# Performance work log

Measured on AMD Instinct MI355X. Metric: run time of the kernel, lower is better.

## Reference

```python
import jax, jax.numpy as jnp
import numpy as np

B, T, I, H, C, L = 64, 256, 256, 1024, 1000, 2


def setup_inputs() -> dict:
    key = jax.random.key(0)
    ks = jax.random.split(key, 10)
    stdv = 1.0 / np.sqrt(H)
    u = lambda k, shape: jax.random.uniform(k, shape, jnp.float32, -stdv, stdv)
    return {
        "x": jax.random.normal(ks[0], (B, T, I), jnp.float32),
        # gate order: g (tanh), i, f, o — stacked on leading axis
        "W0x": u(ks[1], (4, I, H)),
        "W0h": u(ks[2], (4, H, H)),
        "b0": u(ks[3], (4, H)),
        "W1x": u(ks[4], (4, H, H)),
        "W1h": u(ks[5], (4, H, H)),
        "b1": u(ks[6], (4, H)),
        "Wo": u(ks[7], (H, C)),
        "bo": u(ks[8], (C,)),
    }


def _cell(x, h, c, Wx, Wh, b):
    # z: [4, B, H] — one fused contraction for the 4 gates
    z = jnp.einsum('bi,gih->gbh', x, Wx) + jnp.einsum('bh,ghk->gbk', h, Wh) + b[:, None, :]
    g = jnp.tanh(z[0])
    i = jax.nn.sigmoid(z[1])
    f = jax.nn.sigmoid(z[2])
    o = jax.nn.sigmoid(z[3])
    c_new = g * i + c * f
    h_new = jnp.tanh(c_new) * o
    return h_new, c_new


def reference(x, W0x, W0h, b0, W1x, W1h, b1, Wo, bo):
    xt = jnp.transpose(x, (1, 0, 2))  # [T, B, I] like x.permute(1,0,2)
    zeros = jnp.zeros((B, H), x.dtype)
    init = (zeros, zeros, zeros, zeros)  # h0, c0, h1, c1

    def step(carry, x_t):
        h0, c0, h1, c1 = carry
        h0, c0 = _cell(x_t, h0, c0, W0x, W0h, b0)
        h1, c1 = _cell(h0, h1, c1, W1x, W1h, b1)
        return (h0, c0, h1, c1), None

    (h0, c0, h1, c1), _ = jax.lax.scan(step, init, xt)
    return jnp.matmul(h1, Wo) + bo
```

## Files before the change

kernel.cpp:

```cpp
#include <hip/hip_runtime.h>
#include <cstddef>

#define B_  64
#define T_  256
#define I_  256
#define H_  1024
#define C_  1000
#define BH_ (B_ * H_)
#define SLOTS_B_ 24

typedef _Float16 f16;
typedef __attribute__((ext_vector_type(8))) _Float16 f16x8;
typedef __attribute__((ext_vector_type(4))) float f32x4;

__device__ __forceinline__ float sigmoid_(float v) { return 1.0f / (1.0f + __expf(-v)); }
__device__ __forceinline__ float tanh_(float v) {
  float e = __expf(-2.0f * fabsf(v));
  float t = (1.0f - e) / (1.0f + e);
  return copysignf(t, v);
}

__device__ __forceinline__ void storeH2(f16* p, float a, float b) {
  union { f16 h[2]; unsigned u; } pk;
  pk.h[0] = (f16)a; pk.h[1] = (f16)b;
  __hip_atomic_store((unsigned*)p, pk.u, __ATOMIC_RELAXED, __HIP_MEMORY_SCOPE_AGENT);
}


__device__ __forceinline__ unsigned ldS(unsigned* p) {
  return __hip_atomic_load(p, __ATOMIC_RELAXED, __HIP_MEMORY_SCOPE_AGENT);
}

__device__ __forceinline__ void waitCtr8(unsigned* base, unsigned tgt) {
  int g = 0;
  for (;;) {
    unsigned mn = 0xffffffffu;
#pragma unroll
    for (int j = 0; j < 8; ++j) {
      unsigned v = ldS(base + j * 32);
      mn = (v < mn) ? v : mn;
    }
    if (mn >= tgt) break;
    __builtin_amdgcn_s_sleep(1);
    if (++g > (1 << 17)) break;
  }
}

template<bool IS_L1>
__device__ __forceinline__ void role_main(
    const f16* __restrict__ x16,
    const float* __restrict__ Wx, const float* __restrict__ Wh,
    const float* __restrict__ bias,
    f16* __restrict__ h0hist, f16* __restrict__ h1hist,
    unsigned* sync, int bid, int nslots, int fmask, int lagD,
    float* zbAll, float* cLDS, float* biasLDS)
{
  constexpr int NKT = IS_L1 ? 16 : 10;
  constexpr int KX  = IS_L1 ? 1024 : 256;

  const int tid  = threadIdx.x;
  const int wv   = tid >> 6;
  const int nh   = wv >> 2;
  const int kq   = wv & 3;
  const int lane = tid & 63;
  const int c16  = lane & 15;
  const int quad = lane >> 4;
  const int rr7  = bid & 127;
  const int mgroup  = rr7 & 1;
  const int ubase   = (rr7 >> 1) * 16;
  const int rowbase = mgroup * 32;

  const int sub = (rr7 >> 1) & 7;
  unsigned* ctrC0 = sync + ((0 * 2 + mgroup) * 8) * 32;
  unsigned* ctrC1 = sync + ((1 * 2 + mgroup) * 8) * 32;
  unsigned* ctrOwn = IS_L1 ? ctrC1 : ctrC0;
  unsigned* arrLine = ctrOwn + sub * 32;

  auto kmap = [&](int ii) -> int {
    if (!IS_L1) return (ii < 2) ? (kq * 2 + ii) * 32 : 256 + (kq * 8 + (ii - 2)) * 32;
    else        return (ii < 8) ? (kq * 8 + ii) * 32 : 1024 + (kq * 8 + (ii - 8)) * 32;
  };

  if (tid < 64) biasLDS[tid] = bias[(size_t)(tid >> 4) * H_ + ubase + (tid & 15)];
  cLDS[tid] = 0.0f;

  f16x8 Wreg[2][NKT];
  {
    f16* zpan = (f16*)zbAll + wv * 1024;
#pragma unroll
    for (int ii = 0; ii < NKT; ++ii) {
      const int kbase = kmap(ii);
#pragma unroll
      for (int rw = 0; rw < 16; ++rw) {
        const int krow  = rw * 2 + (lane >> 5);
        const int col32 = lane & 31;
        const int g = nh * 2 + (col32 >> 4);
        const int u = col32 & 15;
        const int k = kbase + krow;
        float wval = (k < KX) ? Wx[((size_t)g * KX + k) * H_ + ubase + u]
                              : Wh[((size_t)g * H_ + (k - KX)) * H_ + ubase + u];
        zpan[krow * 32 + col32] = (f16)wval;
      }
#pragma unroll
      for (int nt = 0; nt < 2; ++nt) {
        f16x8 f;
#pragma unroll
        for (int j = 0; j < 8; ++j)
          f[j] = zpan[(quad * 8 + j) * 32 + nt * 16 + c16];
        Wreg[nt][ii] = f;
      }
    }
  }
  __syncthreads();

  const int row0 = rowbase + c16;

#pragma unroll 1
  for (int p = 0; p <= T_; ++p) {
    const bool active = IS_L1 ? (p >= 1) : (p < T_);
    const int do_fence = (nslots == 2) ? 1
                        : ((fmask < 0) ? 0 : (((p & fmask) == fmask) ? 1 : 0));

    if (active) {
      const int sp  = p % nslots;
      const int spm = (p - 1 + nslots) % nslots;
      const int spp = (p + 1) % nslots;
      const f16* __restrict__ hA = h0hist + (size_t)sp * BH_;
      const f16* __restrict__ hB = h1hist + (size_t)spm * BH_;
      f16* __restrict__ hdst = IS_L1 ? (h1hist + (size_t)sp  * BH_)
                                     : (h0hist + (size_t)spp * BH_);

      f16x8 Abuf[8][2];
      auto loadTile = [&](int ii, int slot) {
        const int kb = kmap(ii) + quad * 8;
#pragma unroll
        for (int mt2 = 0; mt2 < 2; ++mt2) {
          const int row = row0 + mt2 * 16;
          const f16* src;
          if (!IS_L1) {
            src = (ii < 2) ? (x16 + ((size_t)row * T_ + p) * I_ + kb)
                           : (hA + (size_t)row * H_ + (kb - 256));
          } else {
            src = (ii < 8) ? (hA + (size_t)row * H_ + kb)
                           : (hB + (size_t)row * H_ + (kb - 1024));
          }
          Abuf[slot][mt2] = *(const f16x8*)src;
        }
      };

      f32x4 acc[2][2];
#pragma unroll
      for (int mt2 = 0; mt2 < 2; ++mt2)
#pragma unroll
        for (int nt = 0; nt < 2; ++nt)
          acc[mt2][nt] = (f32x4)0.0f;

      auto mfma4 = [&](int slot, int ii) {
        const f16x8 a0 = Abuf[slot][0];
        const f16x8 a1 = Abuf[slot][1];
        acc[0][0] = __builtin_amdgcn_mfma_f32_16x16x32_f16(a0, Wreg[0][ii], acc[0][0], 0, 0, 0);
        acc[0][1] = __builtin_amdgcn_mfma_f32_16x16x32_f16(a0, Wreg[1][ii], acc[0][1], 0, 0, 0);
        acc[1][0] = __builtin_amdgcn_mfma_f32_16x16x32_f16(a1, Wreg[0][ii], acc[1][0], 0, 0, 0);
        acc[1][1] = __builtin_amdgcn_mfma_f32_16x16x32_f16(a1, Wreg[1][ii], acc[1][1], 0, 0, 0);
      };

      if (!IS_L1) {
        loadTile(0, 0); loadTile(1, 1);
        mfma4(0, 0); mfma4(1, 1);
        if (tid == 0) {
          waitCtr8(ctrC0, 8u * (unsigned)p);
          if (lagD >= 0 && p > lagD) waitCtr8(ctrC1, 8u * (unsigned)(p - lagD));
          if (do_fence) __builtin_amdgcn_fence(__ATOMIC_ACQUIRE, "agent");
        }
        __syncthreads();
#pragma unroll
        for (int ii = 2; ii < 10; ++ii) loadTile(ii, ii - 2);
#pragma unroll
        for (int ii = 2; ii < 10; ++ii) mfma4(ii - 2, ii);
      } else {
        if (tid == 0) {
          waitCtr8(ctrC0, 8u * (unsigned)p);
          if (do_fence) __builtin_amdgcn_fence(__ATOMIC_ACQUIRE, "agent");
        }
        __syncthreads();
#pragma unroll
        for (int ii = 0; ii < 8; ++ii) loadTile(ii, ii);
#pragma unroll
        for (int ii = 0; ii < 8; ++ii) mfma4(ii, ii);
        if (tid == 0) {
          waitCtr8(ctrC1, 8u * (unsigned)p);
          if (do_fence) __builtin_amdgcn_fence(__ATOMIC_ACQUIRE, "agent");
        }
        __syncthreads();
#pragma unroll
        for (int ii = 8; ii < 16; ++ii) loadTile(ii, ii - 8);
#pragma unroll
        for (int ii = 8; ii < 16; ++ii) mfma4(ii - 8, ii);
      }

      float* zw = zbAll + (nh * 4 + kq) * 1024;
#pragma unroll
      for (int mt2 = 0; mt2 < 2; ++mt2)
#pragma unroll
        for (int nt = 0; nt < 2; ++nt)
#pragma unroll
          for (int e = 0; e < 4; ++e)
            zw[(mt2 * 2 + nt) * 256 + (quad * 4 + e) * 16 + c16] = acc[mt2][nt][e];

      __syncthreads();

      {
        const int base = tid * 4;
        const int nh1  = base >> 10;
        const int off  = base & 1023;
        f32x4 s = (f32x4)0.0f;
#pragma unroll
        for (int q = 0; q < 4; ++q)
          s += *(const f32x4*)(zbAll + nh1 * 4096 + q * 1024 + off);
        const int nt1 = (off >> 8) & 1;
        const int c0  = off & 15;
        s += *(const f32x4*)(biasLDS + (nh1 * 2 + nt1) * 16 + c0);
        *(f32x4*)(zbAll + nh1 * 4096 + off) = s;
      }
      __syncthreads();

      {
        const int row = tid >> 4, u = tid & 15;
        const int mt2 = row >> 4, r16 = row & 15;
        const float z0 = zbAll[0 * 4096 + (mt2 * 2 + 0) * 256 + r16 * 16 + u];
        const float z1 = zbAll[0 * 4096 + (mt2 * 2 + 1) * 256 + r16 * 16 + u];
        const float z2 = zbAll[1 * 4096 + (mt2 * 2 + 0) * 256 + r16 * 16 + u];
        const float z3 = zbAll[1 * 4096 + (mt2 * 2 + 1) * 256 + r16 * 16 + u];
        const float cv = cLDS[tid];
        const float gt = tanh_(z0);
        const float iv = sigmoid_(z1);
        const float fv = sigmoid_(z2);
        const float ov = sigmoid_(z3);
        const float cn = gt * iv + cv * fv;
        cLDS[tid] = cn;
        const float hn = tanh_(cn) * ov;
        const float hn_hi = __shfl_down(hn, 1);
        if ((tid & 1) == 0)
          storeH2(hdst + (size_t)(rowbase + row) * H_ + ubase + u, hn, hn_hi);
      }
    }

    __syncthreads();
    if (tid == 0)
      __hip_atomic_fetch_add(arrLine, 1u, __ATOMIC_RELAXED, __HIP_MEMORY_SCOPE_AGENT);
  }
}

__global__ __launch_bounds__(512, 2)
void lstm_persistent(const f16* __restrict__ x16,
                     const float* __restrict__ W0x, const float* __restrict__ W0h, const float* __restrict__ b0,
                     const float* __restrict__ W1x, const float* __restrict__ W1h, const float* __restrict__ b1,
                     f16* h0hist, f16* h1hist, unsigned* sync,
                     int nslots, int fmask, int lagD)
{
  __shared__ float zbAll[8192];
  __shared__ float cLDS[512];
  __shared__ float biasLDS[64];
  const int bid = blockIdx.x;
  if (bid >= 128)
    role_main<true >(x16, W1x, W1h, b1, h0hist, h1hist, sync, bid, nslots, fmask, lagD, zbAll, cLDS, biasLDS);
  else
    role_main<false>(x16, W0x, W0h, b0, h0hist, h1hist, sync, bid, nslots, fmask, lagD, zbAll, cLDS, biasLDS);
}

__global__ void cvt_x(const float* __restrict__ xin, f16* __restrict__ xo)
{
  const int i = (blockIdx.x * 256 + threadIdx.x) * 8;
  const float4 a = *(const float4*)(xin + i);
  const float4 b = *(const float4*)(xin + i + 4);
  f16x8 v;
  v[0] = (f16)a.x; v[1] = (f16)a.y; v[2] = (f16)a.z; v[3] = (f16)a.w;
  v[4] = (f16)b.x; v[5] = (f16)b.y; v[6] = (f16)b.z; v[7] = (f16)b.w;
  *(f16x8*)(xo + i) = v;
}

__global__ void out_gemm(const f16* __restrict__ h1,
                         const float* __restrict__ Wo, const float* __restrict__ bo,
                         float* __restrict__ out)
{
  __shared__ float ht[1024][8];
  const int tid = threadIdx.x;
  const int b0r = blockIdx.y * 4;
  for (int i = tid; i < 4096; i += 128) {
    const int rr = i >> 10, k = i & 1023;
    ht[k][rr] = (float)h1[(size_t)(b0r + rr) * H_ + k];
  }
  __syncthreads();
  const int c = blockIdx.x * 125 + tid;
  if (tid < 125) {
    float a0 = 0.f, a1 = 0.f, a2 = 0.f, a3 = 0.f;
#pragma unroll 4
    for (int k = 0; k < 1024; ++k) {
      const float w = Wo[(size_t)k * C_ + c];
      a0 += ht[k][0] * w;
      a1 += ht[k][1] * w;
      a2 += ht[k][2] * w;
      a3 += ht[k][3] * w;
    }
    const float bb = bo[c];
    out[(size_t)(b0r + 0) * C_ + c] = a0 + bb;
    out[(size_t)(b0r + 1) * C_ + c] = a1 + bb;
    out[(size_t)(b0r + 2) * C_ + c] = a2 + bb;
    out[(size_t)(b0r + 3) * C_ + c] = a3 + bb;
  }
}

extern "C" void kernel_launch(void* const* d_in, const int* in_sizes, int n_in,
                              void* d_out, int out_size, void* d_ws, size_t ws_size,
                              hipStream_t stream)
{
  const float* x   = (const float*)d_in[0];
  const float* W0x = (const float*)d_in[1];
  const float* W0h = (const float*)d_in[2];
  const float* b0  = (const float*)d_in[3];
  const float* W1x = (const float*)d_in[4];
  const float* W1h = (const float*)d_in[5];
  const float* b1  = (const float*)d_in[6];
  const float* Wo  = (const float*)d_in[7];
  const float* bo  = (const float*)d_in[8];

  const size_t slotB = (size_t)BH_ * sizeof(f16);
  const size_t xB    = (size_t)B_ * T_ * I_ * sizeof(f16);
  const size_t needA = 4096 + (size_t)2 * (T_ + 1) * slotB + xB;
  const size_t needB = 4096 + (size_t)2 * SLOTS_B_ * slotB + xB;
  int nslots, fmask, lagD;
  if (ws_size >= needA)      { nslots = T_ + 1;   fmask = -1; lagD = -1; }
  else if (ws_size >= needB) { nslots = SLOTS_B_; fmask = 15; lagD = 7;  }
  else                       { nslots = 2;        fmask = 0;  lagD = 0;  }
  const size_t histB = (size_t)nslots * slotB;

  unsigned* sync  = (unsigned*)d_ws;
  f16* h0hist = (f16*)((char*)d_ws + 4096);
  f16* h1hist = (f16*)((char*)h0hist + histB);
  f16* x16    = (f16*)((char*)h1hist + histB);

  hipMemsetAsync(d_ws, 0, 4096 + slotB, stream);
  hipMemsetAsync(h1hist, 0, slotB, stream);

  hipLaunchKernelGGL(cvt_x, dim3((B_ * T_ * I_) / (256 * 8)), dim3(256), 0, stream, x, x16);

  hipLaunchKernelGGL(lstm_persistent, dim3(256), dim3(512), 0, stream,
                     x16, W0x, W0h, b0, W1x, W1h, b1, h0hist, h1hist, sync,
                     nslots, fmask, lagD);

  f16* h1fin = h1hist + (size_t)(T_ % nslots) * BH_;
  hipLaunchKernelGGL(out_gemm, dim3(8, 16), dim3(128), 0, stream,
                     h1fin, Wo, bo, (float*)d_out);
}
```

Before: 2.542 ms.

## Merge layer-1 dual waits into one combined poll and deepen load buffering

Layer-1 blocks now wait on both the layer-0 and layer-1 counters in a single polling loop before any loads. They then issue all 16 tiles of loads using 10 register slots, instead of two wait/sync phases of 8. This removes one barrier and one wait per step and raises memory-level parallelism. The cost is that overlap of the first-half MFMAs with the second wait is lost. Polling now checks once before sleeping and uses exponential backoff, which adds wake-up latency when the wait runs long.

Result: slower. 2.718 ms (+6.9%).

```diff
diff --git a/kernel.cpp b/kernel.cpp
--- a/kernel.cpp
+++ b/kernel.cpp
@@ -31,18 +31,54 @@
   return __hip_atomic_load(p, __ATOMIC_RELAXED, __HIP_MEMORY_SCOPE_AGENT);
 }
 
+__device__ __forceinline__ void sleepN(int lvl) {
+  switch (lvl) {
+    case 0: __builtin_amdgcn_s_sleep(1); break;
+    case 1: __builtin_amdgcn_s_sleep(2); break;
+    case 2: __builtin_amdgcn_s_sleep(4); break;
+    default: __builtin_amdgcn_s_sleep(8); break;
+  }
+}
+
 __device__ __forceinline__ void waitCtr8(unsigned* base, unsigned tgt) {
-  int g = 0;
+  unsigned mn = 0xffffffffu;
+#pragma unroll
+  for (int j = 0; j < 8; ++j) {
+    unsigned v = ldS(base + j * 32);
+    mn = (v < mn) ? v : mn;
+  }
+  if (mn >= tgt) return;
+  int lvl = 0, g = 0;
   for (;;) {
-    unsigned mn = 0xffffffffu;
+    mn = 0xffffffffu;
 #pragma unroll
     for (int j = 0; j < 8; ++j) {
       unsigned v = ldS(base + j * 32);
       mn = (v < mn) ? v : mn;
     }
     if (mn >= tgt) break;
-    __builtin_amdgcn_s_sleep(1);
+    sleepN(lvl);
+    if (lvl < 3) ++lvl;
     if (++g > (1 << 17)) break;
+  }
+}
+
+__device__ __forceinline__ void waitCtr16(unsigned* b0, unsigned t0,
+                                          unsigned* b1, unsigned t1) {
+  int lvl = 0, g = 0;
+  for (;;) {
+    unsigned m0 = 0xffffffffu, m1 = 0xffffffffu;
+#pragma unroll
+    for (int j = 0; j < 8; ++j) {
+      unsigned v0 = ldS(b0 + j * 32);
+      unsigned v1 = ldS(b1 + j * 32);
+      m0 = (v0 < m0) ? v0 : m0;
+      m1 = (v1 < m1) ? v1 : m1;
+    }
+    if (m0 >= t0 && m1 >= t1) return;
+    sleepN(lvl);
+    if (lvl < 3) ++lvl;
+    if (++g > (1 << 17)) return;
   }
 }
 
@@ -55,8 +91,9 @@
     unsigned* sync, int bid, int nslots, int fmask, int lagD,
     float* zbAll, float* cLDS, float* biasLDS)
 {
-  constexpr int NKT = IS_L1 ? 16 : 10;
-  constexpr int KX  = IS_L1 ? 1024 : 256;
+  constexpr int NKT   = IS_L1 ? 16 : 10;
+  constexpr int KX    = IS_L1 ? 1024 : 256;
+  constexpr int NSLOT = IS_L1 ? 10 : 8;
 
   const int tid  = threadIdx.x;
   const int wv   = tid >> 6;
@@ -73,8 +110,7 @@
   const int sub = (rr7 >> 1) & 7;
   unsigned* ctrC0 = sync + ((0 * 2 + mgroup) * 8) * 32;
   unsigned* ctrC1 = sync + ((1 * 2 + mgroup) * 8) * 32;
-  unsigned* ctrOwn = IS_L1 ? ctrC1 : ctrC0;
-  unsigned* arrLine = ctrOwn + sub * 32;
+  unsigned* arrLine = (IS_L1 ? ctrC1 : ctrC0) + sub * 32;
 
   auto kmap = [&](int ii) -> int {
     if (!IS_L1) return (ii < 2) ? (kq * 2 + ii) * 32 : 256 + (kq * 8 + (ii - 2)) * 32;
@@ -115,6 +151,87 @@
 
   const int row0 = rowbase + c16;
 
+  f32x4 acc[2][2];
+  f16x8 Abuf[NSLOT][2];
+
+  auto zeroAcc = [&]() {
+#pragma unroll
+    for (int mt2 = 0; mt2 < 2; ++mt2)
+#pragma unroll
+      for (int nt = 0; nt < 2; ++nt)
+        acc[mt2][nt] = (f32x4)0.0f;
+  };
+  auto mfma4 = [&](int slot, int ii) {
+    const f16x8 a0 = Abuf[slot][0];
+    const f16x8 a1 = Abuf[slot][1];
+    acc[0][0] = __builtin_amdgcn_mfma_f32_16x16x32_f16(a0, Wreg[0][ii], acc[0][0], 0, 0, 0);
+    acc[0][1] = __builtin_amdgcn_mfma_f32_16x16x32_f16(a0, Wreg[1][ii], acc[0][1], 0, 0, 0);
+    acc[1][0] = __builtin_amdgcn_mfma_f32_16x16x32_f16(a1, Wreg[0][ii], acc[1][0], 0, 0, 0);
+    acc[1][1] = __builtin_amdgcn_mfma_f32_16x16x32_f16(a1, Wreg[1][ii], acc[1][1], 0, 0, 0);
+  };
+  auto loadH = [&](const f16* base, int ii, int slot) {
+    const int kb = kmap(ii) + quad * 8;
+    const int koff = (IS_L1 && ii >= 8) ? (kb - 1024) : (IS_L1 ? kb : (kb - 256));
+#pragma unroll
+    for (int mt2 = 0; mt2 < 2; ++mt2) {
+      const int row = row0 + mt2 * 16;
+      Abuf[slot][mt2] = *(const f16x8*)(base + (size_t)row * H_ + koff);
+    }
+  };
+  auto loadX = [&](int pp, int ii, int slot) {
+    const int kb = kmap(ii) + quad * 8;
+#pragma unroll
+    for (int mt2 = 0; mt2 < 2; ++mt2) {
+      const int row = row0 + mt2 * 16;
+      Abuf[slot][mt2] = *(const f16x8*)(x16 + ((size_t)row * T_ + pp) * I_ + kb);
+    }
+  };
+
+  auto epilogue = [&](f16* hdst) {
+    float* zw = zbAll + (nh * 4 + kq) * 1024;
+#pragma unroll
+    for (int mt2 = 0; mt2 < 2; ++mt2)
+#pragma unroll
+      for (int nt = 0; nt < 2; ++nt)
+#pragma unroll
+        for (int e = 0; e < 4; ++e)
+          zw[(mt2 * 2 + nt) * 256 + (quad * 4 + e) * 16 + c16] = acc[mt2][nt][e];
+    __syncthreads();
+    {
+      const int base = tid * 4;
+      const int nh1  = base >> 10;
+      const int off  = base & 1023;
+      f32x4 s = (f32x4)0.0f;
+#pragma unroll
+      for (int q = 0; q < 4; ++q)
+        s += *(const f32x4*)(zbAll + nh1 * 4096 + q * 1024 + off);
+      const int nt1 = (off >> 8) & 1;
+      const int c0  = off & 15;
+      s += *(const f32x4*)(biasLDS + (nh1 * 2 + nt1) * 16 + c0);
+      *(f32x4*)(zbAll + nh1 * 4096 + off) = s;
+    }
+    __syncthreads();
+    {
+      const int row = tid >> 4, u = tid & 15;
+      const int mt2 = row >> 4, r16 = row & 15;
+      const float z0 = zbAll[0 * 4096 + (mt2 * 2 + 0) * 256 + r16 * 16 + u];
+      const float z1 = zbAll[0 * 4096 + (mt2 * 2 + 1) * 256 + r16 * 16 + u];
+      const float z2 = zbAll[1 * 4096 + (mt2 * 2 + 0) * 256 + r16 * 16 + u];
+      const float z3 = zbAll[1 * 4096 + (mt2 * 2 + 1) * 256 + r16 * 16 + u];
+      const float cv = cLDS[tid];
+      const float gt = tanh_(z0);
+      const float iv = sigmoid_(z1);
+      const float fv = sigmoid_(z2);
+      const float ov = sigmoid_(z3);
+      const float cn = gt * iv + cv * fv;
+      cLDS[tid] = cn;
+      const float hn = tanh_(cn) * ov;
+      const float hn_hi = __shfl_down(hn, 1);
+      if ((tid & 1) == 0)
+        storeH2(hdst + (size_t)(rowbase + row) * H_ + ubase + u, hn, hn_hi);
+    }
+  };
+
 #pragma unroll 1
   for (int p = 0; p <= T_; ++p) {
     const bool active = IS_L1 ? (p >= 1) : (p < T_);
@@ -125,47 +242,10 @@
       const int sp  = p % nslots;
       const int spm = (p - 1 + nslots) % nslots;
       const int spp = (p + 1) % nslots;
-      const f16* __restrict__ hA = h0hist + (size_t)sp * BH_;
-      const f16* __restrict__ hB = h1hist + (size_t)spm * BH_;
-      f16* __restrict__ hdst = IS_L1 ? (h1hist + (size_t)sp  * BH_)
-                                     : (h0hist + (size_t)spp * BH_);
-
-      f16x8 Abuf[8][2];
-      auto loadTile = [&](int ii, int slot) {
-        const int kb = kmap(ii) + quad * 8;
-#pragma unroll
-        for (int mt2 = 0; mt2 < 2; ++mt2) {
-          const int row = row0 + mt2 * 16;
-          const f16* src;
-          if (!IS_L1) {
-            src = (ii < 2) ? (x16 + ((size_t)row * T_ + p) * I_ + kb)
-                           : (hA + (size_t)row * H_ + (kb - 256));
-          } else {
-            src = (ii < 8) ? (hA + (size_t)row * H_ + kb)
-                           : (hB + (size_t)row * H_ + (kb - 1024));
-          }
-          Abuf[slot][mt2] = *(const f16x8*)src;
-        }
-      };
-
-      f32x4 acc[2][2];
-#pragma unroll
-      for (int mt2 = 0; mt2 < 2; ++mt2)
-#pragma unroll
-        for (int nt = 0; nt < 2; ++nt)
-          acc[mt2][nt] = (f32x4)0.0f;
-
-      auto mfma4 = [&](int slot, int ii) {
-        const f16x8 a0 = Abuf[slot][0];
-        const f16x8 a1 = Abuf[slot][1];
-        acc[0][0] = __builtin_amdgcn_mfma_f32_16x16x32_f16(a0, Wreg[0][ii], acc[0][0], 0, 0, 0);
-        acc[0][1] = __builtin_amdgcn_mfma_f32_16x16x32_f16(a0, Wreg[1][ii], acc[0][1], 0, 0, 0);
-        acc[1][0] = __builtin_amdgcn_mfma_f32_16x16x32_f16(a1, Wreg[0][ii], acc[1][0], 0, 0, 0);
-        acc[1][1] = __builtin_amdgcn_mfma_f32_16x16x32_f16(a1, Wreg[1][ii], acc[1][1], 0, 0, 0);
-      };
-
-      if (!IS_L1) {
-        loadTile(0, 0); loadTile(1, 1);
+
+      zeroAcc();
+      if constexpr (!IS_L1) {
+        loadX(p, 0, 0); loadX(p, 1, 1);
         mfma4(0, 0); mfma4(1, 1);
         if (tid == 0) {
           waitCtr8(ctrC0, 8u * (unsigned)p);
@@ -173,75 +253,33 @@
           if (do_fence) __builtin_amdgcn_fence(__ATOMIC_ACQUIRE, "agent");
         }
         __syncthreads();
-#pragma unroll
-        for (int ii = 2; ii < 10; ++ii) loadTile(ii, ii - 2);
+        const f16* hA = h0hist + (size_t)sp * BH_;
+        f16* hdst = h0hist + (size_t)spp * BH_;
+#pragma unroll
+        for (int ii = 2; ii < 10; ++ii) loadH(hA, ii, ii - 2);
 #pragma unroll
         for (int ii = 2; ii < 10; ++ii) mfma4(ii - 2, ii);
+        epilogue(hdst);
       } else {
         if (tid == 0) {
-          waitCtr8(ctrC0, 8u * (unsigned)p);
+          waitCtr16(ctrC0, 8u * (unsigned)p, ctrC1, 8u * (unsigned)p);
           if (do_fence) __builtin_amdgcn_fence(__ATOMIC_ACQUIRE, "agent");
         }
         __syncthreads();
-#pragma unroll
-        for (int ii = 0; ii < 8; ++ii) loadTile(ii, ii);
+        const f16* hA = h0hist + (size_t)sp * BH_;
+        const f16* hB = h1hist + (size_t)spm * BH_;
+        f16* hdst = h1hist + (size_t)sp * BH_;
+#pragma unroll
+        for (int ii = 0; ii < 8; ++ii) loadH(hA, ii, ii);
+        loadH(hB, 8, 8); loadH(hB, 9, 9);
 #pragma unroll
         for (int ii = 0; ii < 8; ++ii) mfma4(ii, ii);
-        if (tid == 0) {
-          waitCtr8(ctrC1, 8u * (unsigned)p);
-          if (do_fence) __builtin_amdgcn_fence(__ATOMIC_ACQUIRE, "agent");
-        }
-        __syncthreads();
-#pragma unroll
-        for (int ii = 8; ii < 16; ++ii) loadTile(ii, ii - 8);
-#pragma unroll
-        for (int ii = 8; ii < 16; ++ii) mfma4(ii - 8, ii);
-      }
-
-      float* zw = zbAll + (nh * 4 + kq) * 1024;
-#pragma unroll
-      for (int mt2 = 0; mt2 < 2; ++mt2)
-#pragma unroll
-        for (int nt = 0; nt < 2; ++nt)
-#pragma unroll
-          for (int e = 0; e < 4; ++e)
-            zw[(mt2 * 2 + nt) * 256 + (quad * 4 + e) * 16 + c16] = acc[mt2][nt][e];
-
-      __syncthreads();
-
-      {
-        const int base = tid * 4;
-        const int nh1  = base >> 10;
-        const int off  = base & 1023;
-        f32x4 s = (f32x4)0.0f;
-#pragma unroll
-        for (int q = 0; q < 4; ++q)
-          s += *(const f32x4*)(zbAll + nh1 * 4096 + q * 1024 + off);
-        const int nt1 = (off >> 8) & 1;
-        const int c0  = off & 15;
-        s += *(const f32x4*)(biasLDS + (nh1 * 2 + nt1) * 16 + c0);
-        *(f32x4*)(zbAll + nh1 * 4096 + off) = s;
-      }
-      __syncthreads();
-
-      {
-        const int row = tid >> 4, u = tid & 15;
-        const int mt2 = row >> 4, r16 = row & 15;
-        const float z0 = zbAll[0 * 4096 + (mt2 * 2 + 0) * 256 + r16 * 16 + u];
-        const float z1 = zbAll[0 * 4096 + (mt2 * 2 + 1) * 256 + r16 * 16 + u];
-        const float z2 = zbAll[1 * 4096 + (mt2 * 2 + 0) * 256 + r16 * 16 + u];
-        const float z3 = zbAll[1 * 4096 + (mt2 * 2 + 1) * 256 + r16 * 16 + u];
-        const float cv = cLDS[tid];
-        const float gt = tanh_(z0);
-        const float iv = sigmoid_(z1);
-        const float fv = sigmoid_(z2);
-        const float ov = sigmoid_(z3);
-        const float cn = gt * iv + cv * fv;
-        cLDS[tid] = cn;
-        const float hn = tanh_(cn) * ov;
-        const float hn_hi = __shfl_down(hn, 1);
-        if ((tid & 1) == 0)
-          storeH2(hdst + (size_t)(rowbase + row) * H_ + ubase + u, hn, hn_hi);
+        loadH(hB, 10, 0); loadH(hB, 11, 1); loadH(hB, 12, 2);
+        loadH(hB, 13, 3); loadH(hB, 14, 4); loadH(hB, 15, 5);
+        mfma4(8, 8); mfma4(9, 9);
+        mfma4(0, 10); mfma4(1, 11); mfma4(2, 12);
+        mfma4(3, 13); mfma4(4, 14); mfma4(5, 15);
+        epilogue(hdst);
       }
     }
 
```
